# Optimization experiments

Measured on AMD Instinct MI355X. Metric: run time of the kernel, lower is better.

The kernel has to match this reference:

```python
import jax, jax.numpy as jnp
import numpy as np

N_NODES = 100000  # static segment count for segment_sum
DEGREE = 2        # polynomial degree of the Laplacian filter


def setup_inputs() -> dict:
    key = jax.random.key(0)
    k1, k2, k3, k4 = jax.random.split(key, 4)
    N, E, C = N_NODES, 1600000, 32
    x = jax.random.normal(k1, (N, C), dtype=jnp.float32)
    weights = jax.random.normal(k2, (1 + DEGREE,), dtype=jnp.float32)
    edge_src = jax.random.randint(k3, (E,), 0, N, dtype=jnp.int32)
    edge_dst = jax.random.randint(k4, (E,), 0, N, dtype=jnp.int32)
    return {"x": x, "weights": weights, "edge_src": edge_src, "edge_dst": edge_dst}


def reference(x, weights, edge_src, edge_dst):
    """y = (w0 * I + w1 * L + ... + w_d * L^d) @ x with L = D - A,
    computed by the recurrence t_k = L @ t_{k-1} (never materializing L^k)."""
    N = N_NODES
    # node degrees: D[i] = number of edges landing on i
    deg = jax.ops.segment_sum(jnp.ones_like(edge_src, dtype=x.dtype), edge_dst,
                              num_segments=N)  # [N]

    def lap_matvec(t):
        # (L @ t)[i] = deg[i] * t[i] - sum_{(s->i) in E} t[s]
        agg = jax.ops.segment_sum(t[edge_src], edge_dst, num_segments=N)  # [N, C]
        return deg[:, None] * t - agg

    y = weights[0] * x
    t = x
    for k in range(1, 1 + DEGREE):  # fixed small loop over polynomial order
        t = lap_matvec(t)
        y = y + weights[k] * t
    return y
```

## Files before the change

### kernel.cpp

```cpp
#include <hip/hip_runtime.h>

#define C 32
#define NT 256
#define BSH 8
#define BNODE 256
#define CAPC 5632
#define SRCMASK 0x1FFFF

typedef float f32x4 __attribute__((ext_vector_type(4)));

__device__ __forceinline__ unsigned int f2bf(float f) {
    unsigned int u = __float_as_uint(f);
    return (u + 0x7FFFu + ((u >> 16) & 1u)) >> 16;
}
__device__ __forceinline__ float bflo(unsigned int u) { return __uint_as_float(u << 16); }
__device__ __forceinline__ float bfhi(unsigned int u) { return __uint_as_float(u & 0xFFFF0000u); }

__global__ __launch_bounds__(1024) void phaseA_cvt(const int* __restrict__ src,
                                                   const int* __restrict__ dst,
                                                   int* __restrict__ cursor,
                                                   int* __restrict__ pk,
                                                   const float* __restrict__ x,
                                                   uint2* __restrict__ xb2,
                                                   int N, int E, int nbuck, int chunk) {
    extern __shared__ int l[];
    int* lcnt = l;
    int* lcur = l + nbuck;
    int tid = threadIdx.x;
    for (int i = tid; i < nbuck; i += 1024) lcnt[i] = 0;
    __syncthreads();
    int base = blockIdx.x * chunk;
    int end  = min(base + chunk, E);
    for (int e = base + tid; e < end; e += 1024)
        atomicAdd(&lcnt[dst[e] >> BSH], 1);
    __syncthreads();
    for (int i = tid; i < nbuck; i += 1024) {
        int c = lcnt[i];
        lcur[i] = i * CAPC + (c ? atomicAdd(&cursor[i], c) : 0);
    }
    __syncthreads();
    for (int e = base + tid; e < end; e += 1024) {
        int d = dst[e];
        int b = d >> BSH;
        int pos = atomicAdd(&lcur[b], 1);
        pk[pos] = src[e] | ((d & (BNODE - 1)) << 17);
    }
    if (xb2 != nullptr) {
        int total = N * 8;
        int gid = blockIdx.x * 1024 + tid;
        int gth = gridDim.x * 1024;
        for (int i = gid; i < total; i += gth) {
            f32x4 v = *(const f32x4*)(x + (size_t)i * 4);
            uint2 r;
            r.x = f2bf(v.x) | (f2bf(v.y) << 16);
            r.y = f2bf(v.z) | (f2bf(v.w) << 16);
            xb2[i] = r;
        }
    }
}

__global__ __launch_bounds__(1024) void phaseB_mv1(int* __restrict__ pk,
                                                   const int* __restrict__ cursor,
                                                   int* __restrict__ row_start,
                                                   int* __restrict__ ideg,
                                                   const uint2* __restrict__ xb2,
                                                   uint2* __restrict__ t1b2, int N) {
    __shared__ int ent[CAPC];
    __shared__ int sorted[CAPC];
    __shared__ int h[BNODE];
    __shared__ int ss[BNODE];
    __shared__ int cur[BNODE];
    int b = blockIdx.x;
    int tid = threadIdx.x;
    int n0 = b << BSH;
    int base = b * CAPC;
    int cnt = min(cursor[b], CAPC);

    if (tid < BNODE) h[tid] = 0;
    __syncthreads();
    for (int i = tid; i < cnt; i += 1024) {
        int en = pk[base + i];
        ent[i] = en;
        atomicAdd(&h[en >> 17], 1);
    }
    __syncthreads();
    int v = 0;
    if (tid < BNODE) { v = h[tid]; ss[tid] = v; }
    __syncthreads();
    for (int off = 1; off < BNODE; off <<= 1) {
        int u = 0;
        if (tid < BNODE && tid >= off) u = ss[tid - off];
        __syncthreads();
        if (tid < BNODE) ss[tid] += u;
        __syncthreads();
    }
    if (tid < BNODE) {
        int exc = ss[tid] - v;
        int n = n0 + tid;
        if (n < N) { row_start[n] = base + exc; ideg[n] = v; }
        cur[tid] = exc;
    }
    __syncthreads();
    for (int i = tid; i < cnt; i += 1024) {
        int en = ent[i];
        int pos = atomicAdd(&cur[en >> 17], 1);
        int s = en & SRCMASK;
        sorted[pos] = s;
        pk[base + pos] = s;
    }
    __syncthreads();

    for (int i = tid; i < BNODE * 8; i += 1024) {
        int r = i >> 3;
        int lq = i & 7;
        int n = n0 + r;
        if (n >= N) continue;
        int hi = ss[r];
        int lo = hi - h[r];
        float a0 = 0.f, a1 = 0.f, a2 = 0.f, a3 = 0.f;
        int j = lo;
        for (; j + 3 < hi; j += 4) {
            int s0 = sorted[j], s1 = sorted[j + 1], s2 = sorted[j + 2], s3 = sorted[j + 3];
            uint2 u0 = xb2[(size_t)s0 * 8 + lq];
            uint2 u1 = xb2[(size_t)s1 * 8 + lq];
            uint2 u2 = xb2[(size_t)s2 * 8 + lq];
            uint2 u3 = xb2[(size_t)s3 * 8 + lq];
            a0 += bflo(u0.x); a1 += bfhi(u0.x); a2 += bflo(u0.y); a3 += bfhi(u0.y);
            a0 += bflo(u1.x); a1 += bfhi(u1.x); a2 += bflo(u1.y); a3 += bfhi(u1.y);
            a0 += bflo(u2.x); a1 += bfhi(u2.x); a2 += bflo(u2.y); a3 += bfhi(u2.y);
            a0 += bflo(u3.x); a1 += bfhi(u3.x); a2 += bflo(u3.y); a3 += bfhi(u3.y);
        }
        for (; j < hi; ++j) {
            uint2 u0 = xb2[(size_t)sorted[j] * 8 + lq];
            a0 += bflo(u0.x); a1 += bfhi(u0.x); a2 += bflo(u0.y); a3 += bfhi(u0.y);
        }
        uint2 xs = xb2[(size_t)n * 8 + lq];
        float fdg = (float)h[r];
        float t0 = fdg * bflo(xs.x) - a0;
        float t1v = fdg * bfhi(xs.x) - a1;
        float t2 = fdg * bflo(xs.y) - a2;
        float t3 = fdg * bfhi(xs.y) - a3;
        uint2 rr;
        rr.x = f2bf(t0) | (f2bf(t1v) << 16);
        rr.y = f2bf(t2) | (f2bf(t3) << 16);
        __builtin_nontemporal_store(rr.x, &((unsigned int*)t1b2)[((size_t)n * 8 + lq) * 2]);
        __builtin_nontemporal_store(rr.y, &((unsigned int*)t1b2)[((size_t)n * 8 + lq) * 2 + 1]);
    }
}

__device__ __forceinline__ void accum_seg(const uint2* __restrict__ arr,
                                          const int* __restrict__ pk,
                                          int lo, int hi, int lq,
                                          float& a0, float& a1, float& a2, float& a3) {
#define ACC4(ux, uy) { a0 += bflo(ux); a1 += bfhi(ux); a2 += bflo(uy); a3 += bfhi(uy); }
    int j = lo;
    for (; j + 7 < hi; j += 8) {
        int s0 = __builtin_nontemporal_load(&pk[j]);
        int s1 = __builtin_nontemporal_load(&pk[j + 1]);
        int s2 = __builtin_nontemporal_load(&pk[j + 2]);
        int s3 = __builtin_nontemporal_load(&pk[j + 3]);
        int s4 = __builtin_nontemporal_load(&pk[j + 4]);
        int s5 = __builtin_nontemporal_load(&pk[j + 5]);
        int s6 = __builtin_nontemporal_load(&pk[j + 6]);
        int s7 = __builtin_nontemporal_load(&pk[j + 7]);
        uint2 u0 = arr[(size_t)s0 * 8 + lq];
        uint2 u1 = arr[(size_t)s1 * 8 + lq];
        uint2 u2 = arr[(size_t)s2 * 8 + lq];
        uint2 u3 = arr[(size_t)s3 * 8 + lq];
        uint2 u4 = arr[(size_t)s4 * 8 + lq];
        uint2 u5 = arr[(size_t)s5 * 8 + lq];
        uint2 u6 = arr[(size_t)s6 * 8 + lq];
        uint2 u7 = arr[(size_t)s7 * 8 + lq];
        ACC4(u0.x, u0.y) ACC4(u1.x, u1.y) ACC4(u2.x, u2.y) ACC4(u3.x, u3.y)
        ACC4(u4.x, u4.y) ACC4(u5.x, u5.y) ACC4(u6.x, u6.y) ACC4(u7.x, u7.y)
    }
    for (; j + 1 < hi; j += 2) {
        int s0 = __builtin_nontemporal_load(&pk[j]);
        int s1 = __builtin_nontemporal_load(&pk[j + 1]);
        uint2 u0 = arr[(size_t)s0 * 8 + lq];
        uint2 u1 = arr[(size_t)s1 * 8 + lq];
        ACC4(u0.x, u0.y) ACC4(u1.x, u1.y)
    }
    if (j < hi) {
        uint2 u0 = arr[(size_t)__builtin_nontemporal_load(&pk[j]) * 8 + lq];
        ACC4(u0.x, u0.y)
    }
#undef ACC4
}

__global__ __launch_bounds__(NT) void gather2_bf(const uint2* __restrict__ xb2,
        const uint2* __restrict__ t1b2, const int* __restrict__ pk,
        const int* __restrict__ row_start, const int* __restrict__ ideg,
        const float* __restrict__ wts, float* __restrict__ y, int N) {
    int g = blockIdx.x * blockDim.x + threadIdx.x;
    int n = g >> 3;
    if (n >= N) return;
    int lq = g & 7;
    int rs = row_start[n];
    int dg = ideg[n];
    float a0 = 0.f, a1 = 0.f, a2 = 0.f, a3 = 0.f;
    accum_seg(t1b2, pk, rs, rs + dg, lq, a0, a1, a2, a3);
    uint2 xs = xb2[(size_t)n * 8 + lq];
    uint2 ts = t1b2[(size_t)n * 8 + lq];
    float w0 = wts[0], w1 = wts[1], w2 = wts[2];
    float fdg = (float)dg;
    float tv0 = bflo(ts.x), tv1 = bfhi(ts.x), tv2 = bflo(ts.y), tv3 = bfhi(ts.y);
    f32x4 r;
    r.x = w0 * bflo(xs.x) + w1 * tv0 + w2 * (fdg * tv0 - a0);
    r.y = w0 * bfhi(xs.x) + w1 * tv1 + w2 * (fdg * tv1 - a1);
    r.z = w0 * bflo(xs.y) + w1 * tv2 + w2 * (fdg * tv2 - a2);
    r.w = w0 * bfhi(xs.y) + w1 * tv3 + w2 * (fdg * tv3 - a3);
    size_t o = (size_t)n * C + lq * 4;
    __builtin_nontemporal_store(r, (f32x4*)(y + o));
}

__global__ __launch_bounds__(1024) void phaseB_sort(int* __restrict__ pk,
        const int* __restrict__ cursor, int* __restrict__ row_start,
        int* __restrict__ ideg, int N) {
    __shared__ int ent[CAPC];
    __shared__ int h[BNODE];
    __shared__ int ss[BNODE];
    __shared__ int cur[BNODE];
    int b = blockIdx.x;
    int tid = threadIdx.x;
    int base = b * CAPC;
    int cnt = min(cursor[b], CAPC);
    if (tid < BNODE) h[tid] = 0;
    __syncthreads();
    for (int i = tid; i < cnt; i += 1024) {
        int en = pk[base + i];
        ent[i] = en;
        atomicAdd(&h[en >> 17], 1);
    }
    __syncthreads();
    int v = 0;
    if (tid < BNODE) { v = h[tid]; ss[tid] = v; }
    __syncthreads();
    for (int off = 1; off < BNODE; off <<= 1) {
        int u = 0;
        if (tid < BNODE && tid >= off) u = ss[tid - off];
        __syncthreads();
        if (tid < BNODE) ss[tid] += u;
        __syncthreads();
    }
    if (tid < BNODE) {
        int exc = ss[tid] - v;
        int n = (b << BSH) + tid;
        if (n < N) { row_start[n] = base + exc; ideg[n] = v; }
        cur[tid] = exc;
    }
    __syncthreads();
    for (int i = tid; i < cnt; i += 1024) {
        int en = ent[i];
        int pos = atomicAdd(&cur[en >> 17], 1);
        pk[base + pos] = en & SRCMASK;
    }
}
__global__ __launch_bounds__(NT) void gather1_f32(const float* __restrict__ x,
        const int* __restrict__ pk, const int* __restrict__ row_start,
        const int* __restrict__ ideg, float* __restrict__ t1, int N) {
    int g = blockIdx.x * blockDim.x + threadIdx.x;
    int n = g >> 5;
    if (n >= N) return;
    int ch = g & 31;
    int rs = row_start[n], dg = ideg[n], re = rs + dg;
    float a0 = 0, a1 = 0, a2 = 0, a3 = 0;
    int j = rs;
    for (; j + 3 < re; j += 4) {
        a0 += x[(size_t)pk[j] * C + ch];     a1 += x[(size_t)pk[j + 1] * C + ch];
        a2 += x[(size_t)pk[j + 2] * C + ch]; a3 += x[(size_t)pk[j + 3] * C + ch];
    }
    for (; j < re; ++j) a0 += x[(size_t)pk[j] * C + ch];
    size_t o = (size_t)n * C + ch;
    t1[o] = (float)dg * x[o] - ((a0 + a1) + (a2 + a3));
}
__global__ __launch_bounds__(NT) void gather2_f32(const float* __restrict__ x,
        const float* __restrict__ t1, const int* __restrict__ pk,
        const int* __restrict__ row_start, const int* __restrict__ ideg,
        const float* __restrict__ wts, float* __restrict__ y, int N) {
    int g = blockIdx.x * blockDim.x + threadIdx.x;
    int n = g >> 5;
    if (n >= N) return;
    int ch = g & 31;
    int rs = row_start[n], dg = ideg[n], re = rs + dg;
    float a0 = 0, a1 = 0, a2 = 0, a3 = 0;
    int j = rs;
    for (; j + 3 < re; j += 4) {
        a0 += t1[(size_t)pk[j] * C + ch];     a1 += t1[(size_t)pk[j + 1] * C + ch];
        a2 += t1[(size_t)pk[j + 2] * C + ch]; a3 += t1[(size_t)pk[j + 3] * C + ch];
    }
    for (; j < re; ++j) a0 += t1[(size_t)pk[j] * C + ch];
    size_t o = (size_t)n * C + ch;
    float tv = t1[o];
    y[o] = wts[0] * x[o] + wts[1] * tv + wts[2] * ((float)dg * tv - ((a0 + a1) + (a2 + a3)));
}

extern "C" void kernel_launch(void* const* d_in, const int* in_sizes, int n_in,
                              void* d_out, int out_size, void* d_ws, size_t ws_size,
                              hipStream_t stream) {
    const float* x    = (const float*)d_in[0];
    const float* wts  = (const float*)d_in[1];
    const int*   esrc = (const int*)d_in[2];
    const int*   edst = (const int*)d_in[3];
    float*       y    = (float*)d_out;

    const int N = in_sizes[0] / C;
    const int E = in_sizes[2];
    const int nbuck = (N + BNODE - 1) >> BSH;
    const int nc = N * C;

    char* p = (char*)d_ws;
    auto align16 = [](size_t s) { return (s + 15) & ~(size_t)15; };
    int* cursor    = (int*)p; p += align16((size_t)nbuck * 4);
    int* row_start = (int*)p; p += align16((size_t)N * 4);
    int* ideg      = (int*)p; p += align16((size_t)N * 4);
    int* pk        = (int*)p; p += align16((size_t)nbuck * CAPC * 4);
    uint2* xb2     = (uint2*)p; p += align16((size_t)nc * 2);
    uint2* t1b2    = (uint2*)p; p += align16((size_t)nc * 2);
    float* t1      = (float*)p;
    bool bf_ok = (size_t)(p - (char*)d_ws) <= ws_size;

    hipMemsetAsync(cursor, 0, (size_t)nbuck * 4, stream);

    const int ABLK = 512;
    const int chunk = (E + ABLK - 1) / ABLK;
    const size_t lds_a = (size_t)nbuck * 2 * 4;

    if (bf_ok) {
        phaseA_cvt<<<ABLK, 1024, lds_a, stream>>>(esrc, edst, cursor, pk, x, xb2,
                                                  N, E, nbuck, chunk);
        phaseB_mv1<<<nbuck, 1024, 0, stream>>>(pk, cursor, row_start, ideg,
                                               xb2, t1b2, N);
        const int gblocks = ((size_t)N * 8 + NT - 1) / NT;
        gather2_bf<<<gblocks, NT, 0, stream>>>(xb2, t1b2, pk, row_start, ideg, wts, y, N);
    } else {
        phaseA_cvt<<<ABLK, 1024, lds_a, stream>>>(esrc, edst, cursor, pk, x, nullptr,
                                                  N, E, nbuck, chunk);
        phaseB_sort<<<nbuck, 1024, 0, stream>>>(pk, cursor, row_start, ideg, N);
        const int gblocks = ((size_t)N * 32 + NT - 1) / NT;
        gather1_f32<<<gblocks, NT, 0, stream>>>(x, pk, row_start, ideg, t1, N);
        gather2_f32<<<gblocks, NT, 0, stream>>>(x, t1, pk, row_start, ideg, wts, y, N);
    }
}
```

Baseline: 169.9 us.

## Replace bucketed LDS sort with global-atomic CSR build and separate matvec kernels

Replaces the two-phase bucket sort (LDS histogram plus per-bucket sort fused with the first matvec) with a straightforward CSR construction: global atomic degree counting fused with bf16 conversion, a blockwise scan with atomic block offsets, and an atomic scatter of sources. The first and second Laplacian matvecs become two simple gather kernels. This removes the fixed bucket capacity and LDS-heavy sort, but relies on many random global atomics and adds kernel launches. The workspace size check and the fp32 fallback are dropped.

After: 337.8 us. 1.99x slower.

```diff
diff --git a/kernel.cpp b/kernel.cpp
--- a/kernel.cpp
+++ b/kernel.cpp
@@ -2,10 +2,6 @@
 
 #define C 32
 #define NT 256
-#define BSH 8
-#define BNODE 256
-#define CAPC 5632
-#define SRCMASK 0x1FFFF
 
 typedef float f32x4 __attribute__((ext_vector_type(4)));
 
@@ -16,135 +12,55 @@
 __device__ __forceinline__ float bflo(unsigned int u) { return __uint_as_float(u << 16); }
 __device__ __forceinline__ float bfhi(unsigned int u) { return __uint_as_float(u & 0xFFFF0000u); }
 
-__global__ __launch_bounds__(1024) void phaseA_cvt(const int* __restrict__ src,
-                                                   const int* __restrict__ dst,
-                                                   int* __restrict__ cursor,
-                                                   int* __restrict__ pk,
-                                                   const float* __restrict__ x,
-                                                   uint2* __restrict__ xb2,
-                                                   int N, int E, int nbuck, int chunk) {
-    extern __shared__ int l[];
-    int* lcnt = l;
-    int* lcur = l + nbuck;
-    int tid = threadIdx.x;
-    for (int i = tid; i < nbuck; i += 1024) lcnt[i] = 0;
-    __syncthreads();
-    int base = blockIdx.x * chunk;
-    int end  = min(base + chunk, E);
-    for (int e = base + tid; e < end; e += 1024)
-        atomicAdd(&lcnt[dst[e] >> BSH], 1);
-    __syncthreads();
-    for (int i = tid; i < nbuck; i += 1024) {
-        int c = lcnt[i];
-        lcur[i] = i * CAPC + (c ? atomicAdd(&cursor[i], c) : 0);
-    }
-    __syncthreads();
-    for (int e = base + tid; e < end; e += 1024) {
-        int d = dst[e];
-        int b = d >> BSH;
-        int pos = atomicAdd(&lcur[b], 1);
-        pk[pos] = src[e] | ((d & (BNODE - 1)) << 17);
-    }
-    if (xb2 != nullptr) {
-        int total = N * 8;
-        int gid = blockIdx.x * 1024 + tid;
-        int gth = gridDim.x * 1024;
-        for (int i = gid; i < total; i += gth) {
-            f32x4 v = *(const f32x4*)(x + (size_t)i * 4);
-            uint2 r;
-            r.x = f2bf(v.x) | (f2bf(v.y) << 16);
-            r.y = f2bf(v.z) | (f2bf(v.w) << 16);
-            xb2[i] = r;
-        }
+__global__ __launch_bounds__(256) void k_deg_cvt(const int* __restrict__ dst,
+                                                 int* __restrict__ ideg,
+                                                 const float* __restrict__ x,
+                                                 uint2* __restrict__ xb2,
+                                                 int N, int E) {
+    int gid = blockIdx.x * 256 + threadIdx.x;
+    int gsz = gridDim.x * 256;
+    for (int e = gid; e < E; e += gsz)
+        atomicAdd(&ideg[dst[e]], 1);
+    int total = N * 8;
+    for (int i = gid; i < total; i += gsz) {
+        f32x4 v = *(const f32x4*)(x + (size_t)i * 4);
+        uint2 r;
+        r.x = f2bf(v.x) | (f2bf(v.y) << 16);
+        r.y = f2bf(v.z) | (f2bf(v.w) << 16);
+        xb2[i] = r;
     }
 }
 
-__global__ __launch_bounds__(1024) void phaseB_mv1(int* __restrict__ pk,
-                                                   const int* __restrict__ cursor,
-                                                   int* __restrict__ row_start,
-                                                   int* __restrict__ ideg,
-                                                   const uint2* __restrict__ xb2,
-                                                   uint2* __restrict__ t1b2, int N) {
-    __shared__ int ent[CAPC];
-    __shared__ int sorted[CAPC];
-    __shared__ int h[BNODE];
-    __shared__ int ss[BNODE];
-    __shared__ int cur[BNODE];
-    int b = blockIdx.x;
+__global__ __launch_bounds__(1024) void k_scan(const int* __restrict__ ideg,
+                                               int* __restrict__ rpos,
+                                               int* __restrict__ gcur, int N) {
+    __shared__ int s[1024];
+    __shared__ int base;
     int tid = threadIdx.x;
-    int n0 = b << BSH;
-    int base = b * CAPC;
-    int cnt = min(cursor[b], CAPC);
-
-    if (tid < BNODE) h[tid] = 0;
+    int n = blockIdx.x * 1024 + tid;
+    int v = (n < N) ? ideg[n] : 0;
+    s[tid] = v;
     __syncthreads();
-    for (int i = tid; i < cnt; i += 1024) {
-        int en = pk[base + i];
-        ent[i] = en;
-        atomicAdd(&h[en >> 17], 1);
-    }
-    __syncthreads();
-    int v = 0;
-    if (tid < BNODE) { v = h[tid]; ss[tid] = v; }
-    __syncthreads();
-    for (int off = 1; off < BNODE; off <<= 1) {
-        int u = 0;
-        if (tid < BNODE && tid >= off) u = ss[tid - off];
+    for (int off = 1; off < 1024; off <<= 1) {
+        int u = (tid >= off) ? s[tid - off] : 0;
         __syncthreads();
-        if (tid < BNODE) ss[tid] += u;
+        s[tid] += u;
         __syncthreads();
     }
-    if (tid < BNODE) {
-        int exc = ss[tid] - v;
-        int n = n0 + tid;
-        if (n < N) { row_start[n] = base + exc; ideg[n] = v; }
-        cur[tid] = exc;
-    }
+    if (tid == 1023) base = atomicAdd(gcur, s[1023]);
     __syncthreads();
-    for (int i = tid; i < cnt; i += 1024) {
-        int en = ent[i];
-        int pos = atomicAdd(&cur[en >> 17], 1);
-        int s = en & SRCMASK;
-        sorted[pos] = s;
-        pk[base + pos] = s;
-    }
-    __syncthreads();
+    if (n < N) rpos[n] = base + s[tid] - v;
+}
 
-    for (int i = tid; i < BNODE * 8; i += 1024) {
-        int r = i >> 3;
-        int lq = i & 7;
-        int n = n0 + r;
-        if (n >= N) continue;
-        int hi = ss[r];
-        int lo = hi - h[r];
-        float a0 = 0.f, a1 = 0.f, a2 = 0.f, a3 = 0.f;
-        int j = lo;
-        for (; j + 3 < hi; j += 4) {
-            int s0 = sorted[j], s1 = sorted[j + 1], s2 = sorted[j + 2], s3 = sorted[j + 3];
-            uint2 u0 = xb2[(size_t)s0 * 8 + lq];
-            uint2 u1 = xb2[(size_t)s1 * 8 + lq];
-            uint2 u2 = xb2[(size_t)s2 * 8 + lq];
-            uint2 u3 = xb2[(size_t)s3 * 8 + lq];
-            a0 += bflo(u0.x); a1 += bfhi(u0.x); a2 += bflo(u0.y); a3 += bfhi(u0.y);
-            a0 += bflo(u1.x); a1 += bfhi(u1.x); a2 += bflo(u1.y); a3 += bfhi(u1.y);
-            a0 += bflo(u2.x); a1 += bfhi(u2.x); a2 += bflo(u2.y); a3 += bfhi(u2.y);
-            a0 += bflo(u3.x); a1 += bfhi(u3.x); a2 += bflo(u3.y); a3 += bfhi(u3.y);
-        }
-        for (; j < hi; ++j) {
-            uint2 u0 = xb2[(size_t)sorted[j] * 8 + lq];
-            a0 += bflo(u0.x); a1 += bfhi(u0.x); a2 += bflo(u0.y); a3 += bfhi(u0.y);
-        }
-        uint2 xs = xb2[(size_t)n * 8 + lq];
-        float fdg = (float)h[r];
-        float t0 = fdg * bflo(xs.x) - a0;
-        float t1v = fdg * bfhi(xs.x) - a1;
-        float t2 = fdg * bflo(xs.y) - a2;
-        float t3 = fdg * bfhi(xs.y) - a3;
-        uint2 rr;
-        rr.x = f2bf(t0) | (f2bf(t1v) << 16);
-        rr.y = f2bf(t2) | (f2bf(t3) << 16);
-        __builtin_nontemporal_store(rr.x, &((unsigned int*)t1b2)[((size_t)n * 8 + lq) * 2]);
-        __builtin_nontemporal_store(rr.y, &((unsigned int*)t1b2)[((size_t)n * 8 + lq) * 2 + 1]);
+__global__ __launch_bounds__(256) void k_scatter(const int* __restrict__ src,
+                                                 const int* __restrict__ dst,
+                                                 int* __restrict__ rpos,
+                                                 int* __restrict__ pk, int E) {
+    int gid = blockIdx.x * 256 + threadIdx.x;
+    int gsz = gridDim.x * 256;
+    for (int e = gid; e < E; e += gsz) {
+        int pos = atomicAdd(&rpos[dst[e]], 1);
+        pk[pos] = src[e];
     }
 }
 
@@ -188,18 +104,48 @@
 #undef ACC4
 }
 
-__global__ __launch_bounds__(NT) void gather2_bf(const uint2* __restrict__ xb2,
-        const uint2* __restrict__ t1b2, const int* __restrict__ pk,
-        const int* __restrict__ row_start, const int* __restrict__ ideg,
-        const float* __restrict__ wts, float* __restrict__ y, int N) {
-    int g = blockIdx.x * blockDim.x + threadIdx.x;
+__global__ __launch_bounds__(NT) void k_mv1(const uint2* __restrict__ xb2,
+                                            const int* __restrict__ pk,
+                                            const int* __restrict__ rpos,
+                                            const int* __restrict__ ideg,
+                                            uint2* __restrict__ t1b2, int N) {
+    int g = blockIdx.x * NT + threadIdx.x;
     int n = g >> 3;
     if (n >= N) return;
     int lq = g & 7;
-    int rs = row_start[n];
     int dg = ideg[n];
+    int hi = rpos[n];
+    int lo = hi - dg;
     float a0 = 0.f, a1 = 0.f, a2 = 0.f, a3 = 0.f;
-    accum_seg(t1b2, pk, rs, rs + dg, lq, a0, a1, a2, a3);
+    accum_seg(xb2, pk, lo, hi, lq, a0, a1, a2, a3);
+    uint2 xs = xb2[(size_t)n * 8 + lq];
+    float fdg = (float)dg;
+    float t0 = fdg * bflo(xs.x) - a0;
+    float t1v = fdg * bfhi(xs.x) - a1;
+    float t2 = fdg * bflo(xs.y) - a2;
+    float t3 = fdg * bfhi(xs.y) - a3;
+    uint2 rr;
+    rr.x = f2bf(t0) | (f2bf(t1v) << 16);
+    rr.y = f2bf(t2) | (f2bf(t3) << 16);
+    t1b2[(size_t)n * 8 + lq] = rr;
+}
+
+__global__ __launch_bounds__(NT) void k_mv2(const uint2* __restrict__ xb2,
+                                            const uint2* __restrict__ t1b2,
+                                            const int* __restrict__ pk,
+                                            const int* __restrict__ rpos,
+                                            const int* __restrict__ ideg,
+                                            const float* __restrict__ wts,
+                                            float* __restrict__ y, int N) {
+    int g = blockIdx.x * NT + threadIdx.x;
+    int n = g >> 3;
+    if (n >= N) return;
+    int lq = g & 7;
+    int dg = ideg[n];
+    int hi = rpos[n];
+    int lo = hi - dg;
+    float a0 = 0.f, a1 = 0.f, a2 = 0.f, a3 = 0.f;
+    accum_seg(t1b2, pk, lo, hi, lq, a0, a1, a2, a3);
     uint2 xs = xb2[(size_t)n * 8 + lq];
     uint2 ts = t1b2[(size_t)n * 8 + lq];
     float w0 = wts[0], w1 = wts[1], w2 = wts[2];
@@ -214,87 +160,6 @@
     __builtin_nontemporal_store(r, (f32x4*)(y + o));
 }
 
-__global__ __launch_bounds__(1024) void phaseB_sort(int* __restrict__ pk,
-        const int* __restrict__ cursor, int* __restrict__ row_start,
-        int* __restrict__ ideg, int N) {
-    __shared__ int ent[CAPC];
-    __shared__ int h[BNODE];
-    __shared__ int ss[BNODE];
-    __shared__ int cur[BNODE];
-    int b = blockIdx.x;
-    int tid = threadIdx.x;
-    int base = b * CAPC;
-    int cnt = min(cursor[b], CAPC);
-    if (tid < BNODE) h[tid] = 0;
-    __syncthreads();
-    for (int i = tid; i < cnt; i += 1024) {
-        int en = pk[base + i];
-        ent[i] = en;
-        atomicAdd(&h[en >> 17], 1);
-    }
-    __syncthreads();
-    int v = 0;
-    if (tid < BNODE) { v = h[tid]; ss[tid] = v; }
-    __syncthreads();
-    for (int off = 1; off < BNODE; off <<= 1) {
-        int u = 0;
-        if (tid < BNODE && tid >= off) u = ss[tid - off];
-        __syncthreads();
-        if (tid < BNODE) ss[tid] += u;
-        __syncthreads();
-    }
-    if (tid < BNODE) {
-        int exc = ss[tid] - v;
-        int n = (b << BSH) + tid;
-        if (n < N) { row_start[n] = base + exc; ideg[n] = v; }
-        cur[tid] = exc;
-    }
-    __syncthreads();
-    for (int i = tid; i < cnt; i += 1024) {
-        int en = ent[i];
-        int pos = atomicAdd(&cur[en >> 17], 1);
-        pk[base + pos] = en & SRCMASK;
-    }
-}
-__global__ __launch_bounds__(NT) void gather1_f32(const float* __restrict__ x,
-        const int* __restrict__ pk, const int* __restrict__ row_start,
-        const int* __restrict__ ideg, float* __restrict__ t1, int N) {
-    int g = blockIdx.x * blockDim.x + threadIdx.x;
-    int n = g >> 5;
-    if (n >= N) return;
-    int ch = g & 31;
-    int rs = row_start[n], dg = ideg[n], re = rs + dg;
-    float a0 = 0, a1 = 0, a2 = 0, a3 = 0;
-    int j = rs;
-    for (; j + 3 < re; j += 4) {
-        a0 += x[(size_t)pk[j] * C + ch];     a1 += x[(size_t)pk[j + 1] * C + ch];
-        a2 += x[(size_t)pk[j + 2] * C + ch]; a3 += x[(size_t)pk[j + 3] * C + ch];
-    }
-    for (; j < re; ++j) a0 += x[(size_t)pk[j] * C + ch];
-    size_t o = (size_t)n * C + ch;
-    t1[o] = (float)dg * x[o] - ((a0 + a1) + (a2 + a3));
-}
-__global__ __launch_bounds__(NT) void gather2_f32(const float* __restrict__ x,
-        const float* __restrict__ t1, const int* __restrict__ pk,
-        const int* __restrict__ row_start, const int* __restrict__ ideg,
-        const float* __restrict__ wts, float* __restrict__ y, int N) {
-    int g = blockIdx.x * blockDim.x + threadIdx.x;
-    int n = g >> 5;
-    if (n >= N) return;
-    int ch = g & 31;
-    int rs = row_start[n], dg = ideg[n], re = rs + dg;
-    float a0 = 0, a1 = 0, a2 = 0, a3 = 0;
-    int j = rs;
-    for (; j + 3 < re; j += 4) {
-        a0 += t1[(size_t)pk[j] * C + ch];     a1 += t1[(size_t)pk[j + 1] * C + ch];
-        a2 += t1[(size_t)pk[j + 2] * C + ch]; a3 += t1[(size_t)pk[j + 3] * C + ch];
-    }
-    for (; j < re; ++j) a0 += t1[(size_t)pk[j] * C + ch];
-    size_t o = (size_t)n * C + ch;
-    float tv = t1[o];
-    y[o] = wts[0] * x[o] + wts[1] * tv + wts[2] * ((float)dg * tv - ((a0 + a1) + (a2 + a3)));
-}
-
 extern "C" void kernel_launch(void* const* d_in, const int* in_sizes, int n_in,
                               void* d_out, int out_size, void* d_ws, size_t ws_size,
                               hipStream_t stream) {
@@ -306,39 +171,27 @@
 
     const int N = in_sizes[0] / C;
     const int E = in_sizes[2];
-    const int nbuck = (N + BNODE - 1) >> BSH;
     const int nc = N * C;
 
     char* p = (char*)d_ws;
     auto align16 = [](size_t s) { return (s + 15) & ~(size_t)15; };
-    int* cursor    = (int*)p; p += align16((size_t)nbuck * 4);
-    int* row_start = (int*)p; p += align16((size_t)N * 4);
-    int* ideg      = (int*)p; p += align16((size_t)N * 4);
-    int* pk        = (int*)p; p += align16((size_t)nbuck * CAPC * 4);
-    uint2* xb2     = (uint2*)p; p += align16((size_t)nc * 2);
-    uint2* t1b2    = (uint2*)p; p += align16((size_t)nc * 2);
-    float* t1      = (float*)p;
-    bool bf_ok = (size_t)(p - (char*)d_ws) <= ws_size;
+    int* ideg  = (int*)p; p += align16((size_t)N * 4);
+    int* gcur  = (int*)p; p += 16;
+    int* rpos  = (int*)p; p += align16((size_t)N * 4);
+    int* pk    = (int*)p; p += align16((size_t)E * 4);
+    uint2* xb2 = (uint2*)p; p += align16((size_t)nc * 2);
+    uint2* t1b2 = (uint2*)p; p += align16((size_t)nc * 2);
+    (void)ws_size;
 
-    hipMemsetAsync(cursor, 0, (size_t)nbuck * 4, stream);
+    hipMemsetAsync(ideg, 0, align16((size_t)N * 4) + 16, stream);
 
-    const int ABLK = 512;
-    const int chunk = (E + ABLK - 1) / ABLK;
-    const size_t lds_a = (size_t)nbuck * 2 * 4;
+    const int EB = 2048;
+    const int nsb = (N + 1023) >> 10;
+    const int gblocks = ((size_t)N * 8 + NT - 1) / NT;
 
-    if (bf_ok) {
-        phaseA_cvt<<<ABLK, 1024, lds_a, stream>>>(esrc, edst, cursor, pk, x, xb2,
-                                                  N, E, nbuck, chunk);
-        phaseB_mv1<<<nbuck, 1024, 0, stream>>>(pk, cursor, row_start, ideg,
-                                               xb2, t1b2, N);
-        const int gblocks = ((size_t)N * 8 + NT - 1) / NT;
-        gather2_bf<<<gblocks, NT, 0, stream>>>(xb2, t1b2, pk, row_start, ideg, wts, y, N);
-    } else {
-        phaseA_cvt<<<ABLK, 1024, lds_a, stream>>>(esrc, edst, cursor, pk, x, nullptr,
-                                                  N, E, nbuck, chunk);
-        phaseB_sort<<<nbuck, 1024, 0, stream>>>(pk, cursor, row_start, ideg, N);
-        const int gblocks = ((size_t)N * 32 + NT - 1) / NT;
-        gather1_f32<<<gblocks, NT, 0, stream>>>(x, pk, row_start, ideg, t1, N);
-        gather2_f32<<<gblocks, NT, 0, stream>>>(x, t1, pk, row_start, ideg, wts, y, N);
-    }
+    k_deg_cvt<<<EB, 256, 0, stream>>>(edst, ideg, x, xb2, N, E);
+    k_scan<<<nsb, 1024, 0, stream>>>(ideg, rpos, gcur, N);
+    k_scatter<<<EB, 256, 0, stream>>>(esrc, edst, rpos, pk, E);
+    k_mv1<<<gblocks, NT, 0, stream>>>(xb2, pk, rpos, ideg, t1b2, N);
+    k_mv2<<<gblocks, NT, 0, stream>>>(xb2, t1b2, pk, rpos, ideg, wts, y, N);
 }
```
